# Optimization experiments

Measured on AMD Instinct MI355X. Metric: run time of the kernel, lower is better.

The kernel has to match this reference:

```python
import jax, jax.numpy as jnp
import numpy as np

N_HEAD = 16
D_MODEL = 1024
D_K = 64
D_V = 64
TEMPER = float(np.power(D_MODEL, 0.5))  # NOTE: source scales by sqrt(d_model), not sqrt(d_k)


def setup_inputs() -> dict:
    key = jax.random.key(0)
    ks = jax.random.split(key, 6)
    B, T = 4, 2048
    q = jax.random.normal(ks[0], (B, T, D_MODEL), dtype=jnp.float32)
    k = jax.random.normal(ks[1], (B, T, D_MODEL), dtype=jnp.float32)
    v = jax.random.normal(ks[2], (B, T, D_MODEL), dtype=jnp.float32)
    # xavier_normal for [out, in] = [n_head*d, d_model]; stored as [d_model, n_head*d] for x @ W
    def xavier(kk, fan_out, fan_in):
        std = float(np.sqrt(2.0 / (fan_in + fan_out)))
        return jax.random.normal(kk, (fan_in, fan_out), dtype=jnp.float32) * std
    W_Q = xavier(ks[3], N_HEAD * D_K, D_MODEL)
    W_K = xavier(ks[4], N_HEAD * D_K, D_MODEL)
    W_V = xavier(ks[5], N_HEAD * D_V, D_MODEL)
    return {"q": q, "k": k, "v": v, "W_Q": W_Q, "W_K": W_K, "W_V": W_V}


def reference(q, k, v, W_Q, W_K, W_V):
    B, Tq, _ = q.shape
    Tk = k.shape[1]
    residual = q
    # project and split heads: [B, T, H, d]
    qh = (q @ W_Q).reshape(B, Tq, N_HEAD, D_K)
    kh = (k @ W_K).reshape(B, Tk, N_HEAD, D_K)
    vh = (v @ W_V).reshape(B, Tk, N_HEAD, D_V)
    # scaled dot-product attention (dropout is identity in eval)
    attn = jnp.einsum('bqhd,bkhd->bhqk', qh, kh) / TEMPER
    attn = jax.nn.softmax(attn, axis=-1)
    out = jnp.einsum('bhqk,bkhd->bqhd', attn, vh).reshape(B, Tq, N_HEAD * D_V)
    return out + residual
```

## Files before the change

### kernel.cpp

```cpp
#include <hip/hip_runtime.h>
#include <cstdint>
#include <cstddef>

typedef __bf16 bf16x8 __attribute__((ext_vector_type(8)));
typedef float f32x4 __attribute__((ext_vector_type(4)));
typedef unsigned short u16;
typedef unsigned int u32;

static constexpr int T = 2048;
static constexpr int DM = 1024;
static constexpr float QSCALE = 0.04508422f;

#define GLOBAL_AS __attribute__((address_space(1)))
#define LDS_AS __attribute__((address_space(3)))

__device__ __forceinline__ void gld_lds16(const u16* g, u16* l) {
  __builtin_amdgcn_global_load_lds((const GLOBAL_AS u32*)g, (LDS_AS u32*)l, 16, 0, 0);
}

__device__ __forceinline__ u16 f2bf(float f) {
  u32 u = __builtin_bit_cast(u32, f);
  u += 0x7fffu + ((u >> 16) & 1u);
  return (u16)(u >> 16);
}

__device__ __forceinline__ u32 pkb(float lo, float hi) {
#if __has_builtin(__builtin_amdgcn_cvt_pk_bf16_f32)
  typedef __bf16 bf16x2 __attribute__((ext_vector_type(2)));
  bf16x2 r = __builtin_amdgcn_cvt_pk_bf16_f32(lo, hi);
  return __builtin_bit_cast(u32, r);
#else
  return __builtin_amdgcn_perm(__builtin_bit_cast(u32, hi),
                               __builtin_bit_cast(u32, lo), 0x07060302u);
#endif
}

__device__ __forceinline__ float fexp2(float x) {
#if __has_builtin(__builtin_amdgcn_exp2f)
  return __builtin_amdgcn_exp2f(x);
#else
  return __builtin_exp2f(x);
#endif
}

__device__ __forceinline__ void pl16swap(u32& a, u32& b) {
  asm("v_permlane16_swap_b32 %0, %1" : "+v"(a), "+v"(b));
}
__device__ __forceinline__ void pl32swap(u32& a, u32& b) {
  asm("v_permlane32_swap_b32 %0, %1" : "+v"(a), "+v"(b));
}

__global__ __launch_bounds__(256) void prep(
    const float* __restrict__ q, const float* __restrict__ k, const float* __restrict__ v,
    u16* __restrict__ oq, u16* __restrict__ ok, u16* __restrict__ ov,
    const float* __restrict__ W0, const float* __restrict__ W1, const float* __restrict__ W2,
    u16* __restrict__ O0, u16* __restrict__ O1, u16* __restrict__ O2) {
  const int bid = blockIdx.x;
  if (bid < 12288) {
    const int zz = bid >> 12;
    const int bx = bid & 4095;
    const float* X = zz == 0 ? q : zz == 1 ? k : v;
    u16* O = zz == 0 ? oq : zz == 1 ? ok : ov;
    const size_t i = ((size_t)bx * 256 + threadIdx.x) * 8;
    float4 a0 = *(const float4*)(X + i), a1 = *(const float4*)(X + i + 4);
    uint4 p;
    p.x = pkb(a0.x, a0.y); p.y = pkb(a0.z, a0.w);
    p.z = pkb(a1.x, a1.y); p.w = pkb(a1.z, a1.w);
    *(uint4*)(O + i) = p;
  } else {
    const int t = bid - 12288;
    const int zz = t >> 8;
    const int rem = t & 255;
    const int k0 = (rem & 15) * 64, n0 = (rem >> 4) * 64;
    const float* W = zz == 0 ? W0 : zz == 1 ? W1 : W2;
    u16* O = zz == 0 ? O0 : zz == 1 ? O1 : O2;
    const float sc = zz == 0 ? QSCALE : 1.0f;
    __shared__ float tile[64][68];
    const int tid = threadIdx.x;
#pragma unroll
    for (int it = 0; it < 4; ++it) {
      int chunk = tid + it * 256;
      int r = chunk >> 4, c4 = (chunk & 15) * 4;
      *(float4*)&tile[r][c4] = *(const float4*)(W + (size_t)(k0 + r) * DM + n0 + c4);
    }
    __syncthreads();
#pragma unroll
    for (int it = 0; it < 4; ++it) {
      int chunk = tid + it * 256;
      int n = chunk >> 4, k4 = (chunk & 15) * 4;
      ushort4 o;
      o.x = f2bf(tile[k4 + 0][n] * sc);
      o.y = f2bf(tile[k4 + 1][n] * sc);
      o.z = f2bf(tile[k4 + 2][n] * sc);
      o.w = f2bf(tile[k4 + 3][n] * sc);
      *(ushort4*)(O + (size_t)(n0 + n) * DM + k0 + k4) = o;
    }
  }
}

__global__ __launch_bounds__(256, 4) void gemm_proj(
    const u16* __restrict__ Xq, const u16* __restrict__ Xk, const u16* __restrict__ Xv,
    const u16* __restrict__ Wq, const u16* __restrict__ Wk, const u16* __restrict__ Wv,
    u16* __restrict__ Oq, u16* __restrict__ Ok, u16* __restrict__ VHt) {
  const int z = blockIdx.y;
  const u16* X = z == 0 ? Xq : z == 1 ? Xk : Xv;
  const u16* Wt = z == 0 ? Wq : z == 1 ? Wk : Wv;
  const int xcd = blockIdx.x & 7, j = blockIdx.x >> 3;
  const int n0 = (j & 7) * 128;
  const int m0 = (xcd * 8 + (j >> 3)) * 128;
  __shared__ u16 Al[128][64];
  __shared__ u16 Bl[128][64];
  const int tid = threadIdx.x, w = tid >> 6, lane = tid & 63;
  const int c16 = lane & 15, quad = lane >> 4;
  const int wm = (w >> 1) * 64, wn = (w & 1) * 64;
  const int rk = lane >> 3;
  const int ck = ((lane & 7) ^ rk) * 8;
  const int swz = c16 & 7;
  f32x4 acc[4][4] = {};
  const u16* ga = X + (size_t)(m0 + w * 32 + rk) * DM + ck;
  const u16* gb = Wt + (size_t)(n0 + w * 32 + rk) * DM + ck;
  for (int kk = 0; kk < 1024; kk += 64) {
    __syncthreads();
#pragma unroll
    for (int i = 0; i < 4; ++i) {
      gld_lds16(ga + kk + (size_t)(i * 8) * DM, &Al[w * 32 + i * 8][0]);
      gld_lds16(gb + kk + (size_t)(i * 8) * DM, &Bl[w * 32 + i * 8][0]);
    }
    __syncthreads();
#pragma unroll
    for (int s = 0; s < 2; ++s) {
      bf16x8 af[4], bfr[4];
#pragma unroll
      for (int t = 0; t < 4; ++t) af[t] = *(const bf16x8*)&Al[wm + t * 16 + c16][((quad + 4 * s) ^ swz) * 8];
#pragma unroll
      for (int t = 0; t < 4; ++t) bfr[t] = *(const bf16x8*)&Bl[wn + t * 16 + c16][((quad + 4 * s) ^ swz) * 8];
#pragma unroll
      for (int mt = 0; mt < 4; ++mt)
#pragma unroll
        for (int nt = 0; nt < 4; ++nt)
          acc[mt][nt] = __builtin_amdgcn_mfma_f32_16x16x32_bf16(af[mt], bfr[nt], acc[mt][nt], 0, 0, 0);
    }
  }
  if (z < 2) {
    u16* O = z == 0 ? Oq : Ok;
#pragma unroll
    for (int mt = 0; mt < 4; ++mt)
#pragma unroll
      for (int nt = 0; nt < 4; ++nt)
#pragma unroll
        for (int r = 0; r < 4; ++r) {
          size_t row = m0 + wm + mt * 16 + quad * 4 + r;
          size_t col = n0 + wn + nt * 16 + c16;
          O[row * DM + col] = f2bf(acc[mt][nt][r]);
        }
  } else {
#pragma unroll
    for (int mt = 0; mt < 4; ++mt)
#pragma unroll
      for (int nt = 0; nt < 4; ++nt) {
        const int row0 = m0 + wm + mt * 16 + quad * 4;
        const int col = n0 + wn + nt * 16 + c16;
        const int bb = row0 >> 11, t0 = row0 & 2047;
        const int hh = col >> 6, dd = col & 63;
        ushort4 o;
        o.x = f2bf(acc[mt][nt][0]);
        o.y = f2bf(acc[mt][nt][1]);
        o.z = f2bf(acc[mt][nt][2]);
        o.w = f2bf(acc[mt][nt][3]);
        *(ushort4*)(VHt + ((size_t)((bb * 16 + hh) * 64 + dd)) * T + t0) = o;
      }
  }
}

__global__ __launch_bounds__(256, 4) void flash_kernel(
    const u16* __restrict__ QH, const u16* __restrict__ KH, const u16* __restrict__ VHt,
    const float* __restrict__ res, float* __restrict__ out) {
  const int blk = blockIdx.x;
  const int x = blk & 7, g = blk >> 3;
  const int bh = x * 8 + (g & 7);
  const int qb = g >> 3;
  const int b = bh >> 4, h = bh & 15;
  const int tid = threadIdx.x, w = tid >> 6, lane = tid & 63;
  const int c16 = lane & 15, quad = lane >> 4;
  const int swzq = c16 & 7;
  __shared__ u16 Kl[2][64][64];
  __shared__ u16 Vt[2][64][64];
  const int qbase = qb * 128 + w * 32;
  bf16x8 bq[2][2];
#pragma unroll
  for (int qi = 0; qi < 2; ++qi) {
    const u16* qp = QH + (size_t)(b * T + qbase + qi * 16 + c16) * DM + h * 64 + quad * 8;
    bq[qi][0] = *(const bf16x8*)qp;
    bq[qi][1] = *(const bf16x8*)(qp + 32);
  }
  f32x4 acc[2][4] = {};
  f32x4 accl[2] = {};
  const u32 one2 = 0x3F803F80u;
  const uint4 onev = {one2, one2, one2, one2};
  const bf16x8 vone = __builtin_bit_cast(bf16x8, onev);
  const int rk = lane >> 3;
  const int ck8 = ((lane & 7) ^ rk) * 8;
  const u16* kg = KH + (size_t)(b * T) * DM + h * 64 + ck8;
  const u16* vg = VHt + ((size_t)bh * 64 + w * 16 + rk) * T + ck8;
  {
    const u16* kg0 = kg + (size_t)(w * 16 + rk) * DM;
    gld_lds16(kg0, &Kl[0][w * 16][0]);
    gld_lds16(kg0 + (size_t)8 * DM, &Kl[0][w * 16 + 8][0]);
    gld_lds16(vg, &Vt[0][w * 16][0]);
    gld_lds16(vg + 8 * T, &Vt[0][w * 16 + 8][0]);
  }
  int cur = 0;
  for (int kt = 0; kt < 32; ++kt) {
    __builtin_amdgcn_s_barrier();
    if (kt < 31) {
      const u16* kg0 = kg + (size_t)((kt + 1) * 64 + w * 16 + rk) * DM;
      gld_lds16(kg0, &Kl[cur ^ 1][w * 16][0]);
      gld_lds16(kg0 + (size_t)8 * DM, &Kl[cur ^ 1][w * 16 + 8][0]);
      const u16* vg0 = vg + (kt + 1) * 64;
      gld_lds16(vg0, &Vt[cur ^ 1][w * 16][0]);
      gld_lds16(vg0 + (size_t)8 * T, &Vt[cur ^ 1][w * 16 + 8][0]);
      asm volatile("s_waitcnt vmcnt(4)" ::: "memory");
    } else {
      asm volatile("s_waitcnt vmcnt(0)" ::: "memory");
    }
    __builtin_amdgcn_s_barrier();
    bf16x8 ap[2][2];
    {
      bf16x8 ak[4][2];
#pragma unroll
      for (int mt = 0; mt < 4; ++mt) {
        const int r = mt * 16 + c16;
        ak[mt][0] = *(const bf16x8*)&Kl[cur][r][(quad ^ swzq) * 8];
        ak[mt][1] = *(const bf16x8*)&Kl[cur][r][((4 + quad) ^ swzq) * 8];
      }
#pragma unroll
      for (int qi = 0; qi < 2; ++qi) {
        u32 d[2][2][2];
#pragma unroll
        for (int mt = 0; mt < 4; ++mt) {
          f32x4 st = {};
          st = __builtin_amdgcn_mfma_f32_16x16x32_bf16(ak[mt][0], bq[qi][0], st, 0, 0, 0);
          st = __builtin_amdgcn_mfma_f32_16x16x32_bf16(ak[mt][1], bq[qi][1], st, 0, 0, 0);
          const float p0 = fexp2(st[0]), p1 = fexp2(st[1]);
          const float p2 = fexp2(st[2]), p3 = fexp2(st[3]);
          d[mt >> 1][mt & 1][0] = pkb(p0, p1);
          d[mt >> 1][mt & 1][1] = pkb(p2, p3);
        }
        pl32swap(d[0][0][0], d[0][1][0]);
        pl32swap(d[0][0][1], d[0][1][1]);
        pl32swap(d[1][0][0], d[1][1][0]);
        pl32swap(d[1][0][1], d[1][1][1]);
        pl16swap(d[0][0][0], d[0][1][0]);
        pl16swap(d[0][0][1], d[0][1][1]);
        pl16swap(d[1][0][0], d[1][1][0]);
        pl16swap(d[1][0][1], d[1][1][1]);
        uint4 a0 = {d[0][0][0], d[0][0][1], d[0][1][0], d[0][1][1]};
        uint4 a1 = {d[1][0][0], d[1][0][1], d[1][1][0], d[1][1][1]};
        ap[qi][0] = __builtin_bit_cast(bf16x8, a0);
        ap[qi][1] = __builtin_bit_cast(bf16x8, a1);
      }
    }
#pragma unroll
    for (int nt = 0; nt < 4; ++nt) {
      const int r = nt * 16 + c16;
      const bf16x8 bv0 = *(const bf16x8*)&Vt[cur][r][(quad ^ swzq) * 8];
      const bf16x8 bv1 = *(const bf16x8*)&Vt[cur][r][((4 + quad) ^ swzq) * 8];
#pragma unroll
      for (int qi = 0; qi < 2; ++qi) {
        acc[qi][nt] = __builtin_amdgcn_mfma_f32_16x16x32_bf16(ap[qi][0], bv0, acc[qi][nt], 0, 0, 0);
        acc[qi][nt] = __builtin_amdgcn_mfma_f32_16x16x32_bf16(ap[qi][1], bv1, acc[qi][nt], 0, 0, 0);
      }
    }
#pragma unroll
    for (int qi = 0; qi < 2; ++qi) {
      accl[qi] = __builtin_amdgcn_mfma_f32_16x16x32_bf16(ap[qi][0], vone, accl[qi], 0, 0, 0);
      accl[qi] = __builtin_amdgcn_mfma_f32_16x16x32_bf16(ap[qi][1], vone, accl[qi], 0, 0, 0);
    }
    cur ^= 1;
  }
#pragma unroll
  for (int qi = 0; qi < 2; ++qi) {
#pragma unroll
    for (int r = 0; r < 4; ++r) {
      const float inv = 1.0f / accl[qi][r];
      const size_t rowbase = (size_t)(b * T + qbase + qi * 16 + quad * 4 + r) * DM + h * 64;
#pragma unroll
      for (int nt = 0; nt < 4; ++nt) {
        const size_t idx = rowbase + nt * 16 + c16;
        out[idx] = acc[qi][nt][r] * inv + res[idx];
      }
    }
  }
}

extern "C" void kernel_launch(void* const* d_in, const int* in_sizes, int n_in,
                              void* d_out, int out_size, void* d_ws, size_t ws_size,
                              hipStream_t stream) {
  const float* q = (const float*)d_in[0];
  const float* k = (const float*)d_in[1];
  const float* v = (const float*)d_in[2];
  const float* WQ = (const float*)d_in[3];
  const float* WK = (const float*)d_in[4];
  const float* WV = (const float*)d_in[5];
  char* ws = (char*)d_ws;
  const size_t PH = (size_t)8192 * 1024 * 2;
  const size_t WT = (size_t)1024 * 1024 * 2;
  u16* XqB = (u16*)d_out;
  u16* XkB = (u16*)d_out + (size_t)8192 * 1024;
  u16* XvB = (u16*)(ws);
  u16* WtQ = (u16*)(ws + PH);
  u16* WtK = (u16*)(ws + PH + WT);
  u16* WtV = (u16*)(ws + PH + 2 * WT);
  u16* QH  = (u16*)(ws + PH + 3 * WT);
  u16* KH  = (u16*)(ws + 2 * PH + 3 * WT);
  u16* VHt = (u16*)(ws + 3 * PH + 3 * WT);

  prep<<<dim3(13056), 256, 0, stream>>>(q, k, v, XqB, XkB, XvB,
                                        WQ, WK, WV, WtQ, WtK, WtV);
  gemm_proj<<<dim3(512, 3), 256, 0, stream>>>(XqB, XkB, XvB, WtQ, WtK, WtV, QH, KH, VHt);
  flash_kernel<<<1024, 256, 0, stream>>>(QH, KH, VHt, q, (float*)d_out);
}
```

Measured before the change: 286.5 us.

## Double-buffer projection GEMM LDS tiles with K=32 steps and async prefetch

Restructures the projection GEMM main loop from single-buffered 64-wide K tiles into double-buffered 32-wide K tiles. The next tile is prefetched with global_load_lds while MFMAs run on the current one, using an explicit vmcnt wait and raw barriers. This hides global load latency behind compute, at the cost of twice as many barrier round trips and a new LDS swizzle pattern. Launch bounds drop from 4 to 3 blocks per SM.

```diff
diff --git a/kernel.cpp b/kernel.cpp
--- a/kernel.cpp
+++ b/kernel.cpp
@@ -98,7 +98,7 @@
   }
 }
 
-__global__ __launch_bounds__(256, 4) void gemm_proj(
+__global__ __launch_bounds__(256, 3) void gemm_proj(
     const u16* __restrict__ Xq, const u16* __restrict__ Xk, const u16* __restrict__ Xv,
     const u16* __restrict__ Wq, const u16* __restrict__ Wk, const u16* __restrict__ Wv,
     u16* __restrict__ Oq, u16* __restrict__ Ok, u16* __restrict__ VHt) {
@@ -108,38 +108,47 @@
   const int xcd = blockIdx.x & 7, j = blockIdx.x >> 3;
   const int n0 = (j & 7) * 128;
   const int m0 = (xcd * 8 + (j >> 3)) * 128;
-  __shared__ u16 Al[128][64];
-  __shared__ u16 Bl[128][64];
+  __shared__ u16 Al[2][128][32];
+  __shared__ u16 Bl[2][128][32];
   const int tid = threadIdx.x, w = tid >> 6, lane = tid & 63;
   const int c16 = lane & 15, quad = lane >> 4;
   const int wm = (w >> 1) * 64, wn = (w & 1) * 64;
-  const int rk = lane >> 3;
-  const int ck = ((lane & 7) ^ rk) * 8;
-  const int swz = c16 & 7;
+  const int srow = lane >> 2;
+  const int sk = ((lane & 3) ^ ((lane >> 3) & 3)) * 8;
+  const int rswz = (c16 >> 1) & 3;
   f32x4 acc[4][4] = {};
-  const u16* ga = X + (size_t)(m0 + w * 32 + rk) * DM + ck;
-  const u16* gb = Wt + (size_t)(n0 + w * 32 + rk) * DM + ck;
-  for (int kk = 0; kk < 1024; kk += 64) {
-    __syncthreads();
-#pragma unroll
-    for (int i = 0; i < 4; ++i) {
-      gld_lds16(ga + kk + (size_t)(i * 8) * DM, &Al[w * 32 + i * 8][0]);
-      gld_lds16(gb + kk + (size_t)(i * 8) * DM, &Bl[w * 32 + i * 8][0]);
-    }
-    __syncthreads();
-#pragma unroll
-    for (int s = 0; s < 2; ++s) {
-      bf16x8 af[4], bfr[4];
-#pragma unroll
-      for (int t = 0; t < 4; ++t) af[t] = *(const bf16x8*)&Al[wm + t * 16 + c16][((quad + 4 * s) ^ swz) * 8];
-#pragma unroll
-      for (int t = 0; t < 4; ++t) bfr[t] = *(const bf16x8*)&Bl[wn + t * 16 + c16][((quad + 4 * s) ^ swz) * 8];
-#pragma unroll
-      for (int mt = 0; mt < 4; ++mt)
-#pragma unroll
-        for (int nt = 0; nt < 4; ++nt)
-          acc[mt][nt] = __builtin_amdgcn_mfma_f32_16x16x32_bf16(af[mt], bfr[nt], acc[mt][nt], 0, 0, 0);
-    }
+  const u16* ga = X + (size_t)(m0 + w * 32 + srow) * DM + sk;
+  const u16* gb = Wt + (size_t)(n0 + w * 32 + srow) * DM + sk;
+  gld_lds16(ga, &Al[0][w * 32][0]);
+  gld_lds16(ga + (size_t)16 * DM, &Al[0][w * 32 + 16][0]);
+  gld_lds16(gb, &Bl[0][w * 32][0]);
+  gld_lds16(gb + (size_t)16 * DM, &Bl[0][w * 32 + 16][0]);
+  for (int kt = 0; kt < 32; ++kt) {
+    const int buf = kt & 1;
+    __builtin_amdgcn_s_barrier();
+    if (kt < 31) {
+      const size_t ko = (size_t)(kt + 1) * 32;
+      gld_lds16(ga + ko, &Al[buf ^ 1][w * 32][0]);
+      gld_lds16(ga + ko + (size_t)16 * DM, &Al[buf ^ 1][w * 32 + 16][0]);
+      gld_lds16(gb + ko, &Bl[buf ^ 1][w * 32][0]);
+      gld_lds16(gb + ko + (size_t)16 * DM, &Bl[buf ^ 1][w * 32 + 16][0]);
+      asm volatile("s_waitcnt vmcnt(4)" ::: "memory");
+    } else {
+      asm volatile("s_waitcnt vmcnt(0)" ::: "memory");
+    }
+    __builtin_amdgcn_s_barrier();
+    bf16x8 af[4], bfr[4];
+#pragma unroll
+    for (int t = 0; t < 4; ++t)
+      af[t] = *(const bf16x8*)&Al[buf][wm + t * 16 + c16][(quad ^ rswz) * 8];
+#pragma unroll
+    for (int t = 0; t < 4; ++t)
+      bfr[t] = *(const bf16x8*)&Bl[buf][wn + t * 16 + c16][(quad ^ rswz) * 8];
+#pragma unroll
+    for (int mt = 0; mt < 4; ++mt)
+#pragma unroll
+      for (int nt = 0; nt < 4; ++nt)
+        acc[mt][nt] = __builtin_amdgcn_mfma_f32_16x16x32_bf16(af[mt], bfr[nt], acc[mt][nt], 0, 0, 0);
   }
   if (z < 2) {
     u16* O = z == 0 ? Oq : Ok;
```

New measurement: 288.7 us. No clear change (+0.8%).
